# Performance work log

Hardware: AMD Instinct MI355X
Metric: run time of the kernel (lower is better)

Reference implementation:

```python
import jax, jax.numpy as jnp
import numpy as np

B, S, E, NH = 2, 1024, 2048, 16
DH = E // NH
EPS = 1e-6

def setup_inputs() -> dict:
    key = jax.random.key(0)
    ks = jax.random.split(key, 6)
    q = jax.random.normal(ks[0], (B, S, E), dtype=jnp.float32)
    k = jax.random.normal(ks[1], (B, S, E), dtype=jnp.float32)
    v = jax.random.normal(ks[2], (B, S, E), dtype=jnp.float32)
    Wi = jax.random.normal(ks[3], (3 * E, NH), dtype=jnp.float32) * 0.02
    bi = jax.random.normal(ks[4], (NH,), dtype=jnp.float32) * 0.1
    Wf = jax.random.normal(ks[5], (3 * E, NH), dtype=jnp.float32) * 0.02
    bf = jnp.linspace(3.0, 6.0, NH, dtype=jnp.float32)  # bias_linspace_initializer(3,6)
    ln_scale = jnp.ones((E,), dtype=jnp.float32)
    return {"q": q, "k": k, "v": v, "Wi": Wi, "bi": bi, "Wf": Wf, "bf": bf, "ln_scale": ln_scale}

def _mlstm_forward(q, k, v, Wi, bi, Wf, bf, ln_scale):
    b, s, e = q.shape
    nh = Wi.shape[1]
    dh = e // nh
    x = jnp.concatenate([q, k, v], axis=-1)                     # (B,S,3E)
    ig = (x @ Wi + bi).transpose(0, 2, 1)[..., None]            # (B,NH,S,1)
    fg = (x @ Wf + bf).transpose(0, 2, 1)[..., None]            # (B,NH,S,1)
    split = lambda t: t.reshape(b, s, nh, dh).transpose(0, 2, 1, 3)
    qh, kh, vh = split(q), split(k), split(v)                   # (B,NH,S,DH)
    # parallel_stabilized_simple backend
    log_f = jax.nn.log_sigmoid(fg)                              # (B,NH,S,1)
    log_f_cum = jnp.concatenate(
        [jnp.zeros((b, nh, 1, 1), q.dtype), jnp.cumsum(log_f, axis=2)], axis=2
    )                                                           # (B,NH,S+1,1)
    # D[i,j] = cumsum[i] - cumsum[j] on causal part
    fg_mat = log_f_cum - jnp.transpose(log_f_cum, (0, 1, 3, 2)) # (B,NH,S+1,S+1)
    ltr = jnp.tril(jnp.ones((s, s), dtype=bool))
    log_fg = jnp.where(ltr, fg_mat[:, :, 1:, 1:], -jnp.inf)     # (B,NH,S,S)
    log_D = log_fg + jnp.transpose(ig, (0, 1, 3, 2))            # + i_j per column
    max_log_D = jnp.max(log_D, axis=-1, keepdims=True)          # (B,NH,S,1)
    D = jnp.exp(log_D - max_log_D)
    qk = jnp.einsum('bhsd,bhtd->bhst', qh, kh) / jnp.sqrt(jnp.asarray(dh, q.dtype))
    C = qk * D                                                  # (B,NH,S,S)
    normalizer = jnp.maximum(jnp.abs(C.sum(-1, keepdims=True)), jnp.exp(-max_log_D))
    Cn = C / (normalizer + EPS)
    h = jnp.einsum('bhst,bhtd->bhsd', Cn, vh)                   # (B,NH,S,DH)
    # MultiHeadLayerNorm: normalize over DH per head, scale (no bias)
    mu = h.mean(-1, keepdims=True)
    var = ((h - mu) ** 2).mean(-1, keepdims=True)
    hn = (h - mu) * jax.lax.rsqrt(var + EPS)
    hn = hn * ln_scale.reshape(1, nh, 1, dh)
    return hn.transpose(0, 2, 1, 3).reshape(b, s, e)            # (B,S,E)

def reference(q, k, v, Wi, bi, Wf, bf, ln_scale):
    return _mlstm_forward(q, k, v, Wi, bi, Wf, bf, ln_scale)
```

## Files before the change

### kernel.cpp

```cpp
#include <hip/hip_runtime.h>
#include <hip/hip_bf16.h>

#define B_   2
#define S_   1024
#define E_   2048
#define NH_  16
#define DH_  128
#define EPS_ 1e-6f

using half8   = __attribute__((ext_vector_type(8))) _Float16;
using floatx4 = __attribute__((ext_vector_type(4))) float;

__device__ __forceinline__ half8 cvt8h(const float* __restrict__ p) {
    float4 a = *(const float4*)p;
    float4 b = *(const float4*)(p + 4);
    half8 r;
    r[0] = (_Float16)a.x; r[1] = (_Float16)a.y;
    r[2] = (_Float16)a.z; r[3] = (_Float16)a.w;
    r[4] = (_Float16)b.x; r[5] = (_Float16)b.y;
    r[6] = (_Float16)b.z; r[7] = (_Float16)b.w;
    return r;
}

__global__ __launch_bounds__(256, 4) void gates_kernel(
    const float* __restrict__ q, const float* __restrict__ k,
    const float* __restrict__ v, const float* __restrict__ Wi,
    const float* __restrict__ Wf, float* __restrict__ pre_i,
    float* __restrict__ pre_f)
{
    __shared__ __attribute__((aligned(16))) _Float16 xs[32 * 264];
    __shared__ __attribute__((aligned(16))) _Float16 wt[32 * 264];

    const int t    = threadIdx.x;
    const int w    = t >> 6, lane = t & 63, quad = lane >> 4, l15 = lane & 15;
    const int mw   = w & 1, nw = w >> 1;
    const int m0   = blockIdx.x * 32;
    const int kbase = blockIdx.y * 768;

    floatx4 acc = {0.f, 0.f, 0.f, 0.f};

    for (int c = 0; c < 3; ++c) {
        __syncthreads();
        const int e0   = kbase + c * 256;
        const int tsel = e0 >> 11;
        const int el0  = e0 & 2047;
        const float* xb = (tsel == 0) ? q : (tsel == 1) ? k : v;
        #pragma unroll
        for (int i = 0; i < 4; ++i) {
            int g = t + i * 256;
            int row = g >> 5, grp = g & 31;
            half8 s8 = cvt8h(xb + (size_t)(m0 + row) * E_ + el0 + grp * 8);
            *(half8*)(&xs[row * 264 + grp * 8]) = s8;
        }
        {
            const int kk = t;
            const float* wiRow = Wi + (size_t)(e0 + kk) * NH_;
            const float* wfRow = Wf + (size_t)(e0 + kk) * NH_;
            float wif[16], wff[16];
            #pragma unroll
            for (int i4 = 0; i4 < 4; ++i4) {
                float4 a = *(const float4*)(wiRow + i4 * 4);
                wif[i4*4+0]=a.x; wif[i4*4+1]=a.y; wif[i4*4+2]=a.z; wif[i4*4+3]=a.w;
                float4 b = *(const float4*)(wfRow + i4 * 4);
                wff[i4*4+0]=b.x; wff[i4*4+1]=b.y; wff[i4*4+2]=b.z; wff[i4*4+3]=b.w;
            }
            #pragma unroll
            for (int hh = 0; hh < 16; ++hh) wt[hh * 264 + kk]        = (_Float16)wif[hh];
            #pragma unroll
            for (int hh = 0; hh < 16; ++hh) wt[(16 + hh) * 264 + kk] = (_Float16)wff[hh];
        }
        __syncthreads();
        #pragma unroll
        for (int ks = 0; ks < 8; ++ks) {
            half8 af = *(const half8*)(&xs[(mw * 16 + l15) * 264 + ks * 32 + quad * 8]);
            half8 bw = *(const half8*)(&wt[(nw * 16 + l15) * 264 + ks * 32 + quad * 8]);
            acc = __builtin_amdgcn_mfma_f32_16x16x32_f16(af, bw, acc, 0, 0, 0);
        }
    }
    #pragma unroll
    for (int reg = 0; reg < 4; ++reg) {
        int m   = m0 + mw * 16 + quad * 4 + reg;
        int b   = m >> 10, s = m & 1023;
        int col = nw * 16 + l15;
        float vacc = acc[reg];
        if (col < 16)
            atomicAdd(&pre_i[((size_t)(b * NH_ + col)) * S_ + s], vacc);
        else
            atomicAdd(&pre_f[((size_t)(b * NH_ + col - 16)) * S_ + s], vacc);
    }
}

__global__ void scan_kernel(float* __restrict__ igAj, float* __restrict__ lfCq,
                            float* __restrict__ NFo, const float* __restrict__ bi,
                            const float* __restrict__ bfb)
{
    const int bh   = blockIdx.x;
    const int h    = bh & 15;
    const int lane = threadIdx.x;
    float* igp = igAj + (size_t)bh * S_;
    float* lfp = lfCq + (size_t)bh * S_;
    const float bih = bi[h], bfh = bfb[h];
    float carryF = 0.f, carryM = -3.0e38f;
    float lf_n = lfp[lane], ig_n = igp[lane];
    for (int it = 0; it < 16; ++it) {
        int idx = it * 64 + lane;
        float lf_c = lf_n, ig_c = ig_n;
        if (it < 15) { lf_n = lfp[idx + 64]; ig_n = igp[idx + 64]; }
        float x   = lf_c + bfh;
        float lfv = (x >= 0.f) ? -log1pf(__expf(-x)) : (x - log1pf(__expf(x)));
        float igv = ig_c + bih;
        float sc = lfv;
        #pragma unroll
        for (int off = 1; off < 64; off <<= 1) {
            float o = __shfl_up(sc, off);
            if (lane >= off) sc += o;
        }
        float F = carryF + sc;
        float a = igv - F;
        float ms = a;
        #pragma unroll
        for (int off = 1; off < 64; off <<= 1) {
            float o = __shfl_up(ms, off);
            if (lane >= off) ms = fmaxf(ms, o);
        }
        float M = fmaxf(carryM, ms);
        igp[idx] = a;
        lfp[idx] = -M;
        NFo[(size_t)bh * S_ + idx] = expf(fminf(-(F + M), 80.f));
        carryF = __shfl(F, 63);
        carryM = __shfl(M, 63);
    }
}

__global__ __launch_bounds__(256, 2) void attn_kernel(
    const float* __restrict__ q, const float* __restrict__ k,
    const float* __restrict__ v, const float* __restrict__ Aj,
    const float* __restrict__ Cq, const float* __restrict__ NFi,
    const float* __restrict__ lnsc, float* __restrict__ out)
{
    __shared__ __attribute__((aligned(16))) _Float16 Ks[64 * 136];
    __shared__ __attribute__((aligned(16))) _Float16 Vt[2][128 * 72];
    __shared__ __attribute__((aligned(16))) _Float16 Pb[64 * 72];
    __shared__ float aj[64], ci[64], nfv[64], lns[128];

    const int t    = threadIdx.x;
    const int w    = t >> 6, lane = t & 63, quad = lane >> 4, l15 = lane & 15;
    const int L    = blockIdx.x;
    int qi, bh;
    if (L < 256) { qi = L >> 5;                bh = L & 31; }
    else         { qi = 15 - ((L - 256) >> 5); bh = (L - 256) & 31; }
    const int b    = bh >> 4, h = bh & 15;
    const size_t rowbase = (size_t)b * S_;
    const int q0   = qi * 64;
    const int srow = t >> 4, sgrp = t & 15;

    if (t < 64) {
        ci[t]  = Cq[(size_t)bh * S_ + q0 + t];
        nfv[t] = NFi[(size_t)bh * S_ + q0 + t];
    } else if (t < 192) {
        int d = t - 64;
        lns[d] = lnsc[h * DH_ + d];
    }
    half8 aq[4];
    {
        const float* qrow = q + (rowbase + q0 + w * 16 + l15) * E_ + h * DH_;
        #pragma unroll
        for (int ks = 0; ks < 4; ++ks)
            aq[ks] = cvt8h(qrow + ks * 32 + quad * 8);
    }

    half8 kreg[4], vreg[4];
    float ajreg = 0.f;
    #pragma unroll
    for (int i = 0; i < 4; ++i) {
        size_t goff = (rowbase + (srow + i * 16)) * E_ + h * DH_ + sgrp * 8;
        kreg[i] = cvt8h(k + goff);
        vreg[i] = cvt8h(v + goff);
    }
    if (t < 64) ajreg = Aj[(size_t)bh * S_ + t];

    #pragma unroll
    for (int i = 0; i < 4; ++i) {
        int row = srow + i * 16;
        *(half8*)(&Ks[row * 136 + sgrp * 8]) = kreg[i];
        #pragma unroll
        for (int uu = 0; uu < 8; ++uu) {
            int u = (uu + lane) & 7;
            Vt[0][(sgrp * 8 + u) * 72 + row] = vreg[i][u];
        }
    }
    if (t < 64) aj[t] = ajreg;
    __syncthreads();

    float ci_r[4];
    #pragma unroll
    for (int reg = 0; reg < 4; ++reg) ci_r[reg] = ci[w * 16 + quad * 4 + reg];

    floatx4 acc_h[8];
    #pragma unroll
    for (int i = 0; i < 8; ++i) acc_h[i] = (floatx4){0.f, 0.f, 0.f, 0.f};
    float lrun[4] = {0.f, 0.f, 0.f, 0.f};
    const float rscale = 0.08838834764831845f;

    for (int kt = 0; kt <= qi; ++kt) {
        const int vb = kt & 1;
        if (kt < qi) {
            const int j0n = (kt + 1) * 64;
            #pragma unroll
            for (int i = 0; i < 4; ++i) {
                size_t goff = (rowbase + j0n + (srow + i * 16)) * E_ + h * DH_ + sgrp * 8;
                kreg[i] = cvt8h(k + goff);
                vreg[i] = cvt8h(v + goff);
            }
            if (t < 64) ajreg = Aj[(size_t)bh * S_ + j0n + t];
        }

        floatx4 sacc[4];
        #pragma unroll
        for (int nt = 0; nt < 4; ++nt) sacc[nt] = (floatx4){0.f, 0.f, 0.f, 0.f};
        #pragma unroll
        for (int ks = 0; ks < 4; ++ks) {
            #pragma unroll
            for (int nt = 0; nt < 4; ++nt) {
                half8 bk = *(const half8*)(&Ks[(nt * 16 + l15) * 136 + ks * 32 + quad * 8]);
                sacc[nt] = __builtin_amdgcn_mfma_f32_16x16x32_f16(aq[ks], bk, sacc[nt], 0, 0, 0);
            }
        }
        const bool diag = (kt == qi);
        #pragma unroll
        for (int nt = 0; nt < 4; ++nt) {
            int jl = nt * 16 + l15;
            float a_j = aj[jl];
            #pragma unroll
            for (int reg = 0; reg < 4; ++reg) {
                int rl = w * 16 + quad * 4 + reg;
                float p = 0.f;
                if (!diag || (jl <= rl))
                    p = sacc[nt][reg] * rscale * __expf(fminf(ci_r[reg] + a_j, 0.f));
                lrun[reg] += p;
                Pb[rl * 72 + jl] = (_Float16)p;
            }
        }
        __syncthreads();

        #pragma unroll
        for (int ks2 = 0; ks2 < 2; ++ks2) {
            half8 ap = *(const half8*)(&Pb[(w * 16 + l15) * 72 + ks2 * 32 + quad * 8]);
            #pragma unroll
            for (int nt2 = 0; nt2 < 8; ++nt2) {
                half8 bv = *(const half8*)(&Vt[vb][(nt2 * 16 + l15) * 72 + ks2 * 32 + quad * 8]);
                acc_h[nt2] = __builtin_amdgcn_mfma_f32_16x16x32_f16(ap, bv, acc_h[nt2], 0, 0, 0);
            }
        }

        if (kt < qi) {
            #pragma unroll
            for (int i = 0; i < 4; ++i) {
                int row = srow + i * 16;
                *(half8*)(&Ks[row * 136 + sgrp * 8]) = kreg[i];
                #pragma unroll
                for (int uu = 0; uu < 8; ++uu) {
                    int u = (uu + lane) & 7;
                    Vt[vb ^ 1][(sgrp * 8 + u) * 72 + row] = vreg[i][u];
                }
            }
            if (t < 64) aj[t] = ajreg;
            __syncthreads();
        }
    }

    #pragma unroll
    for (int reg = 0; reg < 4; ++reg) {
        float l = lrun[reg];
        #pragma unroll
        for (int off = 1; off < 16; off <<= 1) l += __shfl_xor(l, off);
        int rl = w * 16 + quad * 4 + reg;
        float nrm = fmaxf(fabsf(l), nfv[rl]) + EPS_;
        float inv = 1.f / nrm;
        float hv[8];
        float sum = 0.f, sq = 0.f;
        #pragma unroll
        for (int nt2 = 0; nt2 < 8; ++nt2) {
            float x = acc_h[nt2][reg] * inv;
            hv[nt2] = x; sum += x; sq += x * x;
        }
        #pragma unroll
        for (int off = 1; off < 16; off <<= 1) {
            sum += __shfl_xor(sum, off);
            sq  += __shfl_xor(sq, off);
        }
        float mean = sum * (1.f / 128.f);
        float var  = fmaxf(sq * (1.f / 128.f) - mean * mean, 0.f);
        float rstd = rsqrtf(var + EPS_);
        size_t orow = (rowbase + q0 + rl) * E_ + h * DH_;
        #pragma unroll
        for (int nt2 = 0; nt2 < 8; ++nt2) {
            int d = nt2 * 16 + l15;
            out[orow + d] = (hv[nt2] - mean) * rstd * lns[d];
        }
    }
}

extern "C" void kernel_launch(void* const* d_in, const int* in_sizes, int n_in,
                              void* d_out, int out_size, void* d_ws, size_t ws_size,
                              hipStream_t stream)
{
    const float* q    = (const float*)d_in[0];
    const float* k    = (const float*)d_in[1];
    const float* v    = (const float*)d_in[2];
    const float* Wi   = (const float*)d_in[3];
    const float* bi   = (const float*)d_in[4];
    const float* Wf   = (const float*)d_in[5];
    const float* bfb  = (const float*)d_in[6];
    const float* lnsc = (const float*)d_in[7];
    float* out        = (float*)d_out;

    const int NS = B_ * NH_ * S_;
    float* igAj = (float*)d_ws;
    float* lfCq = igAj + NS;
    float* NFa  = lfCq + NS;

    hipMemsetAsync(d_ws, 0, 2 * (size_t)NS * sizeof(float), stream);
    gates_kernel<<<dim3(64, 8), 256, 0, stream>>>(q, k, v, Wi, Wf, igAj, lfCq);
    scan_kernel<<<dim3(32), 64, 0, stream>>>(igAj, lfCq, NFa, bi, bfb);
    attn_kernel<<<dim3(512), 256, 0, stream>>>(q, k, v, igAj, lfCq, NFa, lnsc, out);
}
```

Measured before the change: 180.3 us.

## Replace gate atomics and memset with split-K partial buffers; defer K/V conversion

The gates kernel now writes each of its 8 K-split partial sums to a separate slice instead of using atomicAdd into a zeroed buffer. The scan kernel sums the 8 partials itself, which removes the hipMemsetAsync launch and the atomic contention. Separately, the attention kernel prefetches K/V as raw float4 and converts to fp16 only when storing to LDS, so load latency overlaps with compute. This holds more registers live across the loop and uses more workspace.

```diff
diff --git a/kernel.cpp b/kernel.cpp
--- a/kernel.cpp
+++ b/kernel.cpp
@@ -21,6 +21,14 @@
     r[6] = (_Float16)b.z; r[7] = (_Float16)b.w;
     return r;
 }
+__device__ __forceinline__ half8 cvt2f4(float4 a, float4 b) {
+    half8 r;
+    r[0] = (_Float16)a.x; r[1] = (_Float16)a.y;
+    r[2] = (_Float16)a.z; r[3] = (_Float16)a.w;
+    r[4] = (_Float16)b.x; r[5] = (_Float16)b.y;
+    r[6] = (_Float16)b.z; r[7] = (_Float16)b.w;
+    return r;
+}
 
 __global__ __launch_bounds__(256, 4) void gates_kernel(
     const float* __restrict__ q, const float* __restrict__ k,
@@ -35,7 +43,8 @@
     const int w    = t >> 6, lane = t & 63, quad = lane >> 4, l15 = lane & 15;
     const int mw   = w & 1, nw = w >> 1;
     const int m0   = blockIdx.x * 32;
-    const int kbase = blockIdx.y * 768;
+    const int by   = blockIdx.y;
+    const int kbase = by * 768;
 
     floatx4 acc = {0.f, 0.f, 0.f, 0.f};
 
@@ -84,31 +93,32 @@
         int col = nw * 16 + l15;
         float vacc = acc[reg];
         if (col < 16)
-            atomicAdd(&pre_i[((size_t)(b * NH_ + col)) * S_ + s], vacc);
+            pre_i[((size_t)(by * 32 + b * NH_ + col)) * S_ + s] = vacc;
         else
-            atomicAdd(&pre_f[((size_t)(b * NH_ + col - 16)) * S_ + s], vacc);
-    }
-}
-
-__global__ void scan_kernel(float* __restrict__ igAj, float* __restrict__ lfCq,
+            pre_f[((size_t)(by * 32 + b * NH_ + col - 16)) * S_ + s] = vacc;
+    }
+}
+
+__global__ void scan_kernel(const float* __restrict__ pre_i,
+                            const float* __restrict__ pre_f,
+                            float* __restrict__ Aj, float* __restrict__ Cq,
                             float* __restrict__ NFo, const float* __restrict__ bi,
                             const float* __restrict__ bfb)
 {
     const int bh   = blockIdx.x;
     const int h    = bh & 15;
     const int lane = threadIdx.x;
-    float* igp = igAj + (size_t)bh * S_;
-    float* lfp = lfCq + (size_t)bh * S_;
     const float bih = bi[h], bfh = bfb[h];
     float carryF = 0.f, carryM = -3.0e38f;
-    float lf_n = lfp[lane], ig_n = igp[lane];
     for (int it = 0; it < 16; ++it) {
         int idx = it * 64 + lane;
-        float lf_c = lf_n, ig_c = ig_n;
-        if (it < 15) { lf_n = lfp[idx + 64]; ig_n = igp[idx + 64]; }
-        float x   = lf_c + bfh;
+        float igv = bih, x = bfh;
+        #pragma unroll
+        for (int y = 0; y < 8; ++y) {
+            igv += pre_i[((size_t)(y * 32 + bh)) * S_ + idx];
+            x   += pre_f[((size_t)(y * 32 + bh)) * S_ + idx];
+        }
         float lfv = (x >= 0.f) ? -log1pf(__expf(-x)) : (x - log1pf(__expf(x)));
-        float igv = ig_c + bih;
         float sc = lfv;
         #pragma unroll
         for (int off = 1; off < 64; off <<= 1) {
@@ -124,9 +134,10 @@
             if (lane >= off) ms = fmaxf(ms, o);
         }
         float M = fmaxf(carryM, ms);
-        igp[idx] = a;
-        lfp[idx] = -M;
-        NFo[(size_t)bh * S_ + idx] = expf(fminf(-(F + M), 80.f));
+        size_t o = (size_t)bh * S_ + idx;
+        Aj[o]  = a;
+        Cq[o]  = -M;
+        NFo[o] = expf(fminf(-(F + M), 80.f));
         carryF = __shfl(F, 63);
         carryM = __shfl(M, 63);
     }
@@ -169,24 +180,26 @@
             aq[ks] = cvt8h(qrow + ks * 32 + quad * 8);
     }
 
-    half8 kreg[4], vreg[4];
+    float4 kraw[4][2], vraw[4][2];
     float ajreg = 0.f;
     #pragma unroll
     for (int i = 0; i < 4; ++i) {
-        size_t goff = (rowbase + (srow + i * 16)) * E_ + h * DH_ + sgrp * 8;
-        kreg[i] = cvt8h(k + goff);
-        vreg[i] = cvt8h(v + goff);
+        const float* gp = k + (rowbase + (srow + i * 16)) * E_ + h * DH_ + sgrp * 8;
+        kraw[i][0] = *(const float4*)gp;  kraw[i][1] = *(const float4*)(gp + 4);
+        const float* vp = v + (rowbase + (srow + i * 16)) * E_ + h * DH_ + sgrp * 8;
+        vraw[i][0] = *(const float4*)vp;  vraw[i][1] = *(const float4*)(vp + 4);
     }
     if (t < 64) ajreg = Aj[(size_t)bh * S_ + t];
 
     #pragma unroll
     for (int i = 0; i < 4; ++i) {
         int row = srow + i * 16;
-        *(half8*)(&Ks[row * 136 + sgrp * 8]) = kreg[i];
+        *(half8*)(&Ks[row * 136 + sgrp * 8]) = cvt2f4(kraw[i][0], kraw[i][1]);
+        half8 vh = cvt2f4(vraw[i][0], vraw[i][1]);
         #pragma unroll
         for (int uu = 0; uu < 8; ++uu) {
             int u = (uu + lane) & 7;
-            Vt[0][(sgrp * 8 + u) * 72 + row] = vreg[i][u];
+            Vt[0][(sgrp * 8 + u) * 72 + row] = vh[u];
         }
     }
     if (t < 64) aj[t] = ajreg;
@@ -208,9 +221,10 @@
             const int j0n = (kt + 1) * 64;
             #pragma unroll
             for (int i = 0; i < 4; ++i) {
-                size_t goff = (rowbase + j0n + (srow + i * 16)) * E_ + h * DH_ + sgrp * 8;
-                kreg[i] = cvt8h(k + goff);
-                vreg[i] = cvt8h(v + goff);
+                const float* gp = k + (rowbase + j0n + (srow + i * 16)) * E_ + h * DH_ + sgrp * 8;
+                kraw[i][0] = *(const float4*)gp;  kraw[i][1] = *(const float4*)(gp + 4);
+                const float* vp = v + (rowbase + j0n + (srow + i * 16)) * E_ + h * DH_ + sgrp * 8;
+                vraw[i][0] = *(const float4*)vp;  vraw[i][1] = *(const float4*)(vp + 4);
             }
             if (t < 64) ajreg = Aj[(size_t)bh * S_ + j0n + t];
         }
@@ -257,11 +271,12 @@
             #pragma unroll
             for (int i = 0; i < 4; ++i) {
                 int row = srow + i * 16;
-                *(half8*)(&Ks[row * 136 + sgrp * 8]) = kreg[i];
+                *(half8*)(&Ks[row * 136 + sgrp * 8]) = cvt2f4(kraw[i][0], kraw[i][1]);
+                half8 vh = cvt2f4(vraw[i][0], vraw[i][1]);
                 #pragma unroll
                 for (int uu = 0; uu < 8; ++uu) {
                     int u = (uu + lane) & 7;
-                    Vt[vb ^ 1][(sgrp * 8 + u) * 72 + row] = vreg[i][u];
+                    Vt[vb ^ 1][(sgrp * 8 + u) * 72 + row] = vh[u];
                 }
             }
             if (t < 64) aj[t] = ajreg;
@@ -315,13 +330,14 @@
     const float* lnsc = (const float*)d_in[7];
     float* out        = (float*)d_out;
 
-    const int NS = B_ * NH_ * S_;
-    float* igAj = (float*)d_ws;
-    float* lfCq = igAj + NS;
-    float* NFa  = lfCq + NS;
-
-    hipMemsetAsync(d_ws, 0, 2 * (size_t)NS * sizeof(float), stream);
-    gates_kernel<<<dim3(64, 8), 256, 0, stream>>>(q, k, v, Wi, Wf, igAj, lfCq);
-    scan_kernel<<<dim3(32), 64, 0, stream>>>(igAj, lfCq, NFa, bi, bfb);
-    attn_kernel<<<dim3(512), 256, 0, stream>>>(q, k, v, igAj, lfCq, NFa, lnsc, out);
-}
+    const int NS  = B_ * NH_ * S_;
+    float* pre_i = (float*)d_ws;
+    float* pre_f = pre_i + 8 * NS;
+    float* Aj    = pre_f + 8 * NS;
+    float* Cq    = Aj + NS;
+    float* NFa   = Cq + NS;
+
+    gates_kernel<<<dim3(64, 8), 256, 0, stream>>>(q, k, v, Wi, Wf, pre_i, pre_f);
+    scan_kernel<<<dim3(32), 64, 0, stream>>>(pre_i, pre_f, Aj, Cq, NFa, bi, bfb);
+    attn_kernel<<<dim3(512), 256, 0, stream>>>(q, k, v, Aj, Cq, NFa, lnsc, out);
+}
```

Measured after the change: 201.8 us. 11.9% more time.
